# Performance work log

Hardware: AMD Instinct MI355X
Metric: run time of the kernel (lower is better)

Reference implementation:

```python
import jax, jax.numpy as jnp
import numpy as np

N_HEADS = 12
HEAD_DIM = 32
H_OUT = 28
W_OUT = 28
EPS_LN = 1e-6
EPS_TS = 1e-6


def _layer_norm(x, g, eps=EPS_LN):
    mu = jnp.mean(x, axis=-1, keepdims=True)
    xc = x - mu
    var = jnp.mean(xc * xc, axis=-1, keepdims=True)
    return xc * jax.lax.rsqrt(var + eps) * g


def setup_inputs() -> dict:
    key = jax.random.key(0)
    ks = jax.random.split(key, 6)
    b, hh, ww, d = 4, 56, 56, 384
    nc = 2 * H_OUT * W_OUT  # 1568
    s = 0.02
    return {
        "x": jax.random.normal(ks[0], (b, hh, ww, d), jnp.float32),
        "clusters": jax.random.normal(ks[1], (b, nc, d), jnp.float32),
        "g1": jnp.ones((d,), jnp.float32),
        "Wq": jax.random.normal(ks[2], (d, d), jnp.float32) * s,
        "Wkv": jax.random.normal(ks[3], (d, 2 * d), jnp.float32) * s,
        "Wo": jax.random.normal(ks[4], (d, d), jnp.float32) * s,
        "res_scale": jnp.ones((d,), jnp.float32),
        "g2": jnp.ones((2 * d,), jnp.float32),
        "Wproj": jax.random.normal(ks[5], (2 * d, 768), jnp.float32) * s,
    }


def reference(x, clusters, g1, Wq, Wkv, Wo, res_scale, g2, Wproj):
    b, hh, ww, d = x.shape
    n = hh * ww
    nc = clusters.shape[1]
    dh = HEAD_DIM
    scale = dh ** -0.5

    xf = x.reshape(b, n, d)
    xn = _layer_norm(xf, g1)
    cn = _layer_norm(clusters, g1)

    # projections; rearrange 'b n (h d) -> b h n d' and 'b n (k h d) -> k b h n d'
    q = (cn @ Wq).reshape(b, nc, N_HEADS, dh).transpose(0, 2, 1, 3)
    kv = (xn @ Wkv).reshape(b, n, 2, N_HEADS, dh)
    k = kv[:, :, 0].transpose(0, 2, 1, 3)  # [b h n dh]
    v = kv[:, :, 1].transpose(0, 2, 1, 3)

    attn = jnp.einsum('bhqd,bhkd->bhqk', q, k) * scale  # [b h nc n]
    # soft assignment: softmax over the query (cluster) axis
    attn = jax.nn.softmax(attn, axis=-2)
    token_sizes = attn.sum(-1)  # [b h nc]
    attn = attn / (token_sizes[..., None] + EPS_TS)
    token_sizes = token_sizes.mean(1)  # [b nc]

    c2 = jnp.einsum('bhqk,bhkd->bhqd', attn, v)
    c2 = c2.transpose(0, 2, 1, 3).reshape(b, nc, d) @ Wo

    token_sizes = token_sizes.reshape(b, nc // 2, 2).sum(-1)  # [b n']

    y = clusters * res_scale + c2
    y = y.reshape(b, nc // 2, 2 * d)  # 'b (n two) d -> b n (two d)'
    y = _layer_norm(y, g2) @ Wproj
    y = y.reshape(b, H_OUT, W_OUT, -1)
    token_sizes = token_sizes.reshape(b, H_OUT, W_OUT)
    return y, token_sizes
```

## Files before the change

### kernel.cpp

```cpp
#include <hip/hip_runtime.h>
#include <hip/hip_bf16.h>

typedef __hip_bfloat16 bf16;
typedef __attribute__((ext_vector_type(8))) short short8;
typedef __attribute__((ext_vector_type(4))) short short4v;
typedef __attribute__((ext_vector_type(4))) float f32x4;

#define B 4
#define NT 3136
#define NC 1568
#define NP 784
#define DMODEL 384
#define D2 768
#define NH 12
#define DH 32
#define SCALE 0.17677669529663687f
#define EPS_LN 1e-6f
#define EPS_TS 1e-6f

__device__ __forceinline__ unsigned short f2bf(float f) {
  return (unsigned short)(__bfloat16_as_ushort(__float2bfloat16(f)));
}
__device__ __forceinline__ float b2f(unsigned short u) {
  return __uint_as_float(((unsigned int)u) << 16);
}

__device__ __forceinline__ float lda(const void* __restrict__ p, size_t i,
                                     int mode, bool inf32) {
  bool f32 = (mode == 2) || (mode == 1 && inf32);
  return f32 ? ((const float*)p)[i]
             : __bfloat162float(((const bf16*)p)[i]);
}
__device__ __forceinline__ float4 lda4(const void* __restrict__ p, size_t i,
                                       int mode, bool inf32) {
  bool f32 = (mode == 2) || (mode == 1 && inf32);
  if (f32) return *(const float4*)((const float*)p + i);
  ushort4 u = *(const ushort4*)((const bf16*)p + i);
  return make_float4(b2f(u.x), b2f(u.y), b2f(u.z), b2f(u.w));
}

__global__ void sniff_kernel(const unsigned short* __restrict__ g1,
                             int* __restrict__ flag) {
  if (threadIdx.x == 0 && blockIdx.x == 0)
    *flag = (g1[0] == 0x3F80) ? 0 : 1;
}

__global__ void transpose_kernel(const void* __restrict__ in,
                                 const int* __restrict__ dtf,
                                 bf16* __restrict__ out, int K, int N) {
  bool inf32 = (*dtf != 0);
  __shared__ float t[32][33];
  int n0 = blockIdx.x * 32, k0 = blockIdx.y * 32;
  int tx = threadIdx.x & 31, ty = threadIdx.x >> 5;
#pragma unroll
  for (int s = 0; s < 32; s += 8)
    t[ty + s][tx] = lda(in, (size_t)(k0 + ty + s) * N + n0 + tx, 1, inf32);
  __syncthreads();
#pragma unroll
  for (int s = 0; s < 32; s += 8)
    out[(size_t)(n0 + ty + s) * K + k0 + tx] = __float2bfloat16(t[tx][ty + s]);
}

__global__ void stats_kernel(const void* __restrict__ in, int mode,
                             const int* __restrict__ dtf,
                             float* __restrict__ stats, int D) {
  bool inf32 = (*dtf != 0);
  int row = blockIdx.x;
  int tid = threadIdx.x;
  size_t base = (size_t)row * D;
  int nper = D >> 7;
  float s = 0.f, s2 = 0.f;
  for (int i = 0; i < nper; i++) {
    float xv = lda(in, base + tid + (i << 7), mode, inf32);
    s += xv; s2 += xv * xv;
  }
  __shared__ float red[128], red2[128];
  red[tid] = s; red2[tid] = s2;
  __syncthreads();
  for (int off = 64; off > 0; off >>= 1) {
    if (tid < off) { red[tid] += red[tid + off]; red2[tid] += red2[tid + off]; }
    __syncthreads();
  }
  if (tid == 0) {
    float mean = red[0] / (float)D;
    float var  = red2[0] / (float)D - mean * mean;
    stats[row * 2]     = mean;
    stats[row * 2 + 1] = rsqrtf(var + EPS_LN);
  }
}

__global__ void __launch_bounds__(256, 3)
mgemm_kernel(const void* __restrict__ A, int a_mode, size_t a_bstr,
             const float* __restrict__ Astats, size_t s_bstr,
             const void* __restrict__ gammaA,
             const bf16* __restrict__ BT,
             const int* __restrict__ dtf,
             void* __restrict__ C, int c_f32, size_t c_bstr,
             bf16* __restrict__ Cv,
             int M, int N, int K,
             int epi,
             const void* __restrict__ resid, size_t r_bstr,
             const void* __restrict__ rscale) {
  bool inf32 = (*dtf != 0);
  int z = blockIdx.z;
  size_t a_off = (size_t)z * a_bstr;
  size_t r_off = (size_t)z * r_bstr;
  const float* st = Astats ? Astats + (size_t)z * s_bstr : nullptr;
  __shared__ __align__(16) unsigned short Asl[128][40];
  __shared__ __align__(16) unsigned short Bsl[128][40];
  int tid = threadIdx.x;
  int wave = tid >> 6, lane = tid & 63, l16 = lane & 15, quad = lane >> 4;
  int brow = blockIdx.y * 128, bcol = blockIdx.x * 128;
  int wm = (wave >> 1) * 64, wn = (wave & 1) * 64;
  f32x4 acc[4][4];
#pragma unroll
  for (int i = 0; i < 4; i++)
#pragma unroll
    for (int j = 0; j < 4; j++) acc[i][j] = (f32x4){0.f, 0.f, 0.f, 0.f};

  for (int k0 = 0; k0 < K; k0 += 32) {
#pragma unroll
    for (int it = 0; it < 4; it++) {
      int i = it * 256 + tid;
      int r = i >> 3, c4 = (i & 7) * 4;
      int grow = brow + r;
      if (grow >= M) grow = M - 1;
      float4 v = lda4(A, a_off + (size_t)grow * K + k0 + c4, a_mode, inf32);
      if (st) {
        float mu = st[grow * 2], rstd = st[grow * 2 + 1];
        float4 g = lda4(gammaA, k0 + c4, 1, inf32);
        v.x = (v.x - mu) * rstd * g.x; v.y = (v.y - mu) * rstd * g.y;
        v.z = (v.z - mu) * rstd * g.z; v.w = (v.w - mu) * rstd * g.w;
      }
      ushort4 u = {f2bf(v.x), f2bf(v.y), f2bf(v.z), f2bf(v.w)};
      *(ushort4*)&Asl[r][c4] = u;
    }
#pragma unroll
    for (int it = 0; it < 4; it++) {
      int i = it * 256 + tid;
      int r = i >> 3, c4 = (i & 7) * 4;
      *(ushort4*)&Bsl[r][c4] =
          *(const ushort4*)(BT + (size_t)(bcol + r) * K + k0 + c4);
    }
    __syncthreads();
    short8 af[4], bfr[4];
#pragma unroll
    for (int i = 0; i < 4; i++)
      af[i] = *(const short8*)&Asl[wm + 16 * i + l16][quad * 8];
#pragma unroll
    for (int j = 0; j < 4; j++)
      bfr[j] = *(const short8*)&Bsl[wn + 16 * j + l16][quad * 8];
#pragma unroll
    for (int i = 0; i < 4; i++)
#pragma unroll
      for (int j = 0; j < 4; j++)
        acc[i][j] = __builtin_amdgcn_mfma_f32_16x16x32_bf16(
            af[i], bfr[j], acc[i][j], 0, 0, 0);
    __syncthreads();
  }
#pragma unroll
  for (int i = 0; i < 4; i++) {
#pragma unroll
    for (int r = 0; r < 4; r++) {
      int m = brow + wm + 16 * i + quad * 4 + r;
      if (m < M) {
#pragma unroll
        for (int j = 0; j < 4; j++) {
          int n = bcol + wn + 16 * j + l16;
          float v = acc[i][j][r];
          if (epi == 1)
            v += lda(resid, r_off + (size_t)m * N + n, 1, inf32) *
                 lda(rscale, n, 1, inf32);
          if (epi == 2) {
            if (n < DMODEL) {
              ((bf16*)C)[(size_t)z * c_bstr + (size_t)m * DMODEL + n] =
                  __float2bfloat16(v);
            } else {
              int cc = n - DMODEL, hh = cc >> 5, dd = cc & 31;
              Cv[(((size_t)z * NH + hh) * DH + dd) * NT + m] =
                  __float2bfloat16(v);
            }
          } else {
            size_t idx = (size_t)z * c_bstr + (size_t)m * N + n;
            if (c_f32) ((float*)C)[idx] = v;
            else       ((bf16*)C)[idx]  = __float2bfloat16(v);
          }
        }
      }
    }
  }
}

__global__ void __launch_bounds__(256, 4)
colsum_mfma(const bf16* __restrict__ qm, const bf16* __restrict__ km,
            float* __restrict__ csinv) {
  int b = blockIdx.z, h = blockIdx.y;
  int tid = threadIdx.x;
  int wave = tid >> 6, lane = tid & 63, l16 = lane & 15, quad = lane >> 4;
  int key = blockIdx.x * 64 + wave * 16 + l16;
  short8 kfrag = *(const short8*)(km +
      ((size_t)(b * NT + key) * DMODEL + h * DH + quad * 8));
  __shared__ __align__(16) unsigned short Qlds[32][40];
  const bf16* qb = qm + (size_t)b * NC * DMODEL + h * DH;
  int srow = tid >> 3, sc4 = (tid & 7) * 4;
  float csum = 0.f;
  for (int q0 = 0; q0 < NC; q0 += 32) {
    ushort4 qu = *(const ushort4*)(qb + (size_t)(q0 + srow) * DMODEL + sc4);
    __syncthreads();
    *(ushort4*)&Qlds[srow][sc4] = qu;
    __syncthreads();
    short8 a1 = *(const short8*)&Qlds[l16][quad * 8];
    short8 a2 = *(const short8*)&Qlds[16 + l16][quad * 8];
    f32x4 z = {0.f, 0.f, 0.f, 0.f};
    f32x4 s1 = __builtin_amdgcn_mfma_f32_16x16x32_bf16(a1, kfrag, z, 0, 0, 0);
    f32x4 s2 = __builtin_amdgcn_mfma_f32_16x16x32_bf16(a2, kfrag, z, 0, 0, 0);
#pragma unroll
    for (int r = 0; r < 4; r++)
      csum += __expf(s1[r] * SCALE) + __expf(s2[r] * SCALE);
  }
  csum += __shfl_xor(csum, 16, 64);
  csum += __shfl_xor(csum, 32, 64);
  if (quad == 0)
    csinv[((size_t)b * NH + h) * NT + key] = 1.0f / csum;
}

__global__ void __launch_bounds__(256, 4)
pv_mfma(const bf16* __restrict__ qm, const bf16* __restrict__ km,
        const bf16* __restrict__ vt, const float* __restrict__ csinv,
        bf16* __restrict__ c2, float* __restrict__ rowsum) {
  int b = blockIdx.z, h = blockIdx.y;
  int tid = threadIdx.x;
  int wave = tid >> 6, lane = tid & 63, l16 = lane & 15, quad = lane >> 4;
  int q0w = blockIdx.x * 128 + wave * 32;
  short8 qfrag[2];
#pragma unroll
  for (int t = 0; t < 2; t++) {
    int qr = q0w + t * 16 + l16; if (qr >= NC) qr = NC - 1;
    qfrag[t] = *(const short8*)(qm +
        ((size_t)(b * NC + qr) * DMODEL + h * DH + quad * 8));
  }
  __shared__ __align__(16) unsigned short Klds[64][40];
  __shared__ __align__(16) unsigned short Vlds[32][72];
  __shared__ __align__(16) float csl[64];
  f32x4 olo[2], ohi[2];
#pragma unroll
  for (int t = 0; t < 2; t++) {
    olo[t] = (f32x4){0.f, 0.f, 0.f, 0.f};
    ohi[t] = (f32x4){0.f, 0.f, 0.f, 0.f};
  }
  float rs[2] = {0.f, 0.f};
  const float* csb = csinv + ((size_t)b * NH + h) * NT;
  const bf16* kb = km + (size_t)b * NT * DMODEL + h * DH;
  const bf16* vtb = vt + ((size_t)b * NH + h) * DH * NT;
  int krow = tid >> 2, kc8 = (tid & 3) * 8;
  int vrow = tid >> 3, vc8 = (tid & 7) * 8;
  for (int k0 = 0; k0 < NT; k0 += 64) {
    ushort4 ku0 = *(const ushort4*)(kb + (size_t)(k0 + krow) * DMODEL + kc8);
    ushort4 ku1 = *(const ushort4*)(kb + (size_t)(k0 + krow) * DMODEL + kc8 + 4);
    ushort4 vu0 = *(const ushort4*)(vtb + (size_t)vrow * NT + k0 + vc8);
    ushort4 vu1 = *(const ushort4*)(vtb + (size_t)vrow * NT + k0 + vc8 + 4);
    float4 cf;
    if (tid < 16) cf = *(const float4*)(csb + k0 + tid * 4);
    __syncthreads();
    *(ushort4*)&Klds[krow][kc8] = ku0;
    *(ushort4*)&Klds[krow][kc8 + 4] = ku1;
    *(ushort4*)&Vlds[vrow][vc8] = vu0;
    *(ushort4*)&Vlds[vrow][vc8 + 4] = vu1;
    if (tid < 16) *(float4*)&csl[tid * 4] = cf;
    __syncthreads();
#pragma unroll
    for (int ks = 0; ks < 64; ks += 32) {
      short8 kf1 = *(const short8*)&Klds[ks + l16][quad * 8];
      short8 kf2 = *(const short8*)&Klds[ks + 16 + l16][quad * 8];
      float4 ci1 = *(const float4*)&csl[ks + quad * 4];
      float4 ci2 = *(const float4*)&csl[ks + 16 + quad * 4];
      short4v va = *(const short4v*)&Vlds[l16][ks + quad * 4];
      short4v vb = *(const short4v*)&Vlds[l16][ks + 16 + quad * 4];
      short4v vc = *(const short4v*)&Vlds[16 + l16][ks + quad * 4];
      short4v vd = *(const short4v*)&Vlds[16 + l16][ks + 16 + quad * 4];
      short8 vlo, vhi;
#pragma unroll
      for (int j = 0; j < 4; j++) {
        vlo[j] = va[j]; vlo[4 + j] = vb[j];
        vhi[j] = vc[j]; vhi[4 + j] = vd[j];
      }
#pragma unroll
      for (int t = 0; t < 2; t++) {
        f32x4 z = {0.f, 0.f, 0.f, 0.f};
        f32x4 s1 = __builtin_amdgcn_mfma_f32_16x16x32_bf16(kf1, qfrag[t], z, 0, 0, 0);
        f32x4 s2 = __builtin_amdgcn_mfma_f32_16x16x32_bf16(kf2, qfrag[t], z, 0, 0, 0);
        float p0 = __expf(s1[0] * SCALE) * ci1.x;
        float p1 = __expf(s1[1] * SCALE) * ci1.y;
        float p2 = __expf(s1[2] * SCALE) * ci1.z;
        float p3 = __expf(s1[3] * SCALE) * ci1.w;
        float p4 = __expf(s2[0] * SCALE) * ci2.x;
        float p5 = __expf(s2[1] * SCALE) * ci2.y;
        float p6 = __expf(s2[2] * SCALE) * ci2.z;
        float p7 = __expf(s2[3] * SCALE) * ci2.w;
        rs[t] += ((p0 + p1) + (p2 + p3)) + ((p4 + p5) + (p6 + p7));
        short8 pf;
        pf[0] = (short)f2bf(p0); pf[1] = (short)f2bf(p1);
        pf[2] = (short)f2bf(p2); pf[3] = (short)f2bf(p3);
        pf[4] = (short)f2bf(p4); pf[5] = (short)f2bf(p5);
        pf[6] = (short)f2bf(p6); pf[7] = (short)f2bf(p7);
        olo[t] = __builtin_amdgcn_mfma_f32_16x16x32_bf16(pf, vlo, olo[t], 0, 0, 0);
        ohi[t] = __builtin_amdgcn_mfma_f32_16x16x32_bf16(pf, vhi, ohi[t], 0, 0, 0);
      }
    }
  }
  bf16* c2b = c2 + (size_t)b * NC * DMODEL + h * DH;
#pragma unroll
  for (int t = 0; t < 2; t++) {
    float v = rs[t];
    v += __shfl_xor(v, 16, 64);
    v += __shfl_xor(v, 32, 64);
    rs[t] = v;
#pragma unroll
    for (int r = 0; r < 4; r++) {
      int qloc = quad * 4 + r;
      float rsq = __shfl(rs[t], qloc, 64);
      int q = q0w + t * 16 + qloc;
      if (q < NC) {
        float inv = 1.0f / (rsq + EPS_TS);
        c2b[(size_t)q * DMODEL + l16]      = __float2bfloat16(olo[t][r] * inv);
        c2b[(size_t)q * DMODEL + 16 + l16] = __float2bfloat16(ohi[t][r] * inv);
      }
    }
    int qr = q0w + t * 16 + l16;
    if (quad == 0 && qr < NC)
      rowsum[((size_t)b * NH + h) * NC + qr] = rs[t];
  }
}

__global__ void tok_kernel(const float* __restrict__ rowsum,
                           float* __restrict__ out_ts) {
  int idx = blockIdx.x * 256 + threadIdx.x;
  if (idx >= B * NP) return;
  int b = idx / NP, p = idx % NP;
  float s = 0.f;
  for (int h = 0; h < NH; h++) {
    const float* r = rowsum + ((size_t)b * NH + h) * NC;
    s += r[2 * p] + r[2 * p + 1];
  }
  out_ts[idx] = s / (float)NH;
}

extern "C" void kernel_launch(void* const* d_in, const int* in_sizes, int n_in,
                              void* d_out, int out_size, void* d_ws, size_t ws_size,
                              hipStream_t stream) {
  const void* x         = d_in[0];
  const void* clusters  = d_in[1];
  const void* g1        = d_in[2];
  const void* Wq        = d_in[3];
  const void* Wkv       = d_in[4];
  const void* Wo        = d_in[5];
  const void* res_scale = d_in[6];
  const void* g2        = d_in[7];
  const void* Wproj     = d_in[8];
  float* out = (float*)d_out;

  float* fws = (float*)d_ws;
  size_t fo = 0;
  int*   dtf     = (int*)(fws + fo); fo += 4;
  float* stats_x = fws + fo; fo += (size_t)B * NT * 2;
  float* stats_c = fws + fo; fo += (size_t)B * NC * 2;
  float* stats_y = fws + fo; fo += (size_t)B * NP * 2;
  float* colsum  = fws + fo; fo += (size_t)B * NH * NT;
  float* rowsum  = fws + fo; fo += (size_t)B * NH * NC;
  float* y1f     = fws + fo; fo += (size_t)B * NC * DMODEL;
  fo = (fo + 3) & ~(size_t)3;
  bf16* bws = (bf16*)(fws + fo);
  size_t o = 0;
  bf16* qm     = bws + o; o += (size_t)B * NC * DMODEL;
  bf16* km     = bws + o; o += (size_t)B * NT * DMODEL;
  bf16* vt     = bws + o; o += (size_t)B * NH * DH * NT;
  bf16* c2     = bws + o; o += (size_t)B * NC * DMODEL;
  bf16* wqT    = bws + o; o += (size_t)DMODEL * DMODEL;
  bf16* wkvT   = bws + o; o += (size_t)DMODEL * D2;
  bf16* woT    = bws + o; o += (size_t)DMODEL * DMODEL;
  bf16* wprojT = bws + o; o += (size_t)D2 * D2;

  const size_t xstr = (size_t)NT * DMODEL, cstr = (size_t)NC * DMODEL;
  const size_t ystr = (size_t)NP * D2;

  sniff_kernel<<<1, 1, 0, stream>>>((const unsigned short*)g1, dtf);
  transpose_kernel<<<dim3(DMODEL / 32, DMODEL / 32), 256, 0, stream>>>(
      Wq, dtf, wqT, DMODEL, DMODEL);
  transpose_kernel<<<dim3(D2 / 32, DMODEL / 32), 256, 0, stream>>>(
      Wkv, dtf, wkvT, DMODEL, D2);
  transpose_kernel<<<dim3(DMODEL / 32, DMODEL / 32), 256, 0, stream>>>(
      Wo, dtf, woT, DMODEL, DMODEL);
  transpose_kernel<<<dim3(D2 / 32, D2 / 32), 256, 0, stream>>>(
      Wproj, dtf, wprojT, D2, D2);
  stats_kernel<<<B * NT, 128, 0, stream>>>(x, 1, dtf, stats_x, DMODEL);
  stats_kernel<<<B * NC, 128, 0, stream>>>(clusters, 1, dtf, stats_c, DMODEL);

  mgemm_kernel<<<dim3(DMODEL / 128, (NC + 127) / 128, B), 256, 0, stream>>>(
      clusters, 1, cstr, stats_c, (size_t)NC * 2, g1, wqT, dtf,
      qm, 0, cstr, nullptr, NC, DMODEL, DMODEL, 0, nullptr, 0, nullptr);
  mgemm_kernel<<<dim3(D2 / 128, (NT + 127) / 128, B), 256, 0, stream>>>(
      x, 1, xstr, stats_x, (size_t)NT * 2, g1, wkvT, dtf,
      km, 0, xstr, vt, NT, D2, DMODEL, 2, nullptr, 0, nullptr);
  colsum_mfma<<<dim3(NT / 64, NH, B), 256, 0, stream>>>(qm, km, colsum);
  pv_mfma<<<dim3((NC + 127) / 128, NH, B), 256, 0, stream>>>(
      qm, km, vt, colsum, c2, rowsum);
  mgemm_kernel<<<dim3(DMODEL / 128, (NC + 127) / 128, B), 256, 0, stream>>>(
      c2, 0, cstr, nullptr, 0, nullptr, woT, dtf,
      y1f, 1, cstr, nullptr, NC, DMODEL, DMODEL, 1, clusters, cstr, res_scale);
  stats_kernel<<<B * NP, 128, 0, stream>>>(y1f, 2, dtf, stats_y, D2);
  mgemm_kernel<<<dim3(D2 / 128, (NP + 127) / 128, B), 256, 0, stream>>>(
      y1f, 2, cstr, stats_y, (size_t)NP * 2, g2, wprojT, dtf,
      out, 1, ystr, nullptr, NP, D2, D2, 0, nullptr, 0, nullptr);
  tok_kernel<<<(B * NP + 255) / 256, 256, 0, stream>>>(
      rowsum, out + (size_t)B * NP * D2);
}
```

Before: 443.4 us.

## Fold softmax scale into Wq, use exp2 with log-domain inverse, permute V layout

```diff
diff --git a/kernel.cpp b/kernel.cpp
--- a/kernel.cpp
+++ b/kernel.cpp
@@ -3,7 +3,6 @@
 
 typedef __hip_bfloat16 bf16;
 typedef __attribute__((ext_vector_type(8))) short short8;
-typedef __attribute__((ext_vector_type(4))) short short4v;
 typedef __attribute__((ext_vector_type(4))) float f32x4;
 
 #define B 4
@@ -15,6 +14,7 @@
 #define NH 12
 #define DH 32
 #define SCALE 0.17677669529663687f
+#define LOG2E 1.4426950408889634f
 #define EPS_LN 1e-6f
 #define EPS_TS 1e-6f
 
@@ -47,7 +47,8 @@
 
 __global__ void transpose_kernel(const void* __restrict__ in,
                                  const int* __restrict__ dtf,
-                                 bf16* __restrict__ out, int K, int N) {
+                                 bf16* __restrict__ out, int K, int N,
+                                 float scale) {
   bool inf32 = (*dtf != 0);
   __shared__ float t[32][33];
   int n0 = blockIdx.x * 32, k0 = blockIdx.y * 32;
@@ -58,7 +59,8 @@
   __syncthreads();
 #pragma unroll
   for (int s = 0; s < 32; s += 8)
-    out[(size_t)(n0 + ty + s) * K + k0 + tx] = __float2bfloat16(t[tx][ty + s]);
+    out[(size_t)(n0 + ty + s) * K + k0 + tx] =
+        __float2bfloat16(t[tx][ty + s] * scale);
 }
 
 __global__ void stats_kernel(const void* __restrict__ in, int mode,
@@ -177,7 +179,9 @@
                   __float2bfloat16(v);
             } else {
               int cc = n - DMODEL, hh = cc >> 5, dd = cc & 31;
-              Cv[(((size_t)z * NH + hh) * DH + dd) * NT + m] =
+              int w = m & 31;
+              int pos = ((w >> 2) & 3) * 8 + (w >> 4) * 4 + (w & 3);
+              Cv[(((size_t)z * NH + hh) * DH + dd) * NT + (m & ~31) + pos] =
                   __float2bfloat16(v);
             }
           } else {
@@ -193,17 +197,22 @@
 
 __global__ void __launch_bounds__(256, 4)
 colsum_mfma(const bf16* __restrict__ qm, const bf16* __restrict__ km,
-            float* __restrict__ csinv) {
+            float* __restrict__ l2ci) {
   int b = blockIdx.z, h = blockIdx.y;
   int tid = threadIdx.x;
   int wave = tid >> 6, lane = tid & 63, l16 = lane & 15, quad = lane >> 4;
-  int key = blockIdx.x * 64 + wave * 16 + l16;
-  short8 kfrag = *(const short8*)(km +
-      ((size_t)(b * NT + key) * DMODEL + h * DH + quad * 8));
+  int key0 = blockIdx.x * 128 + wave * 32 + l16;
+  int key1 = key0 + 16;
+  int kc0 = (key0 < NT) ? key0 : NT - 1;
+  int kc1 = (key1 < NT) ? key1 : NT - 1;
+  short8 kf0 = *(const short8*)(km +
+      ((size_t)(b * NT + kc0) * DMODEL + h * DH + quad * 8));
+  short8 kf1 = *(const short8*)(km +
+      ((size_t)(b * NT + kc1) * DMODEL + h * DH + quad * 8));
   __shared__ __align__(16) unsigned short Qlds[32][40];
   const bf16* qb = qm + (size_t)b * NC * DMODEL + h * DH;
   int srow = tid >> 3, sc4 = (tid & 7) * 4;
-  float csum = 0.f;
+  float cs0 = 0.f, cs1 = 0.f;
   for (int q0 = 0; q0 < NC; q0 += 32) {
     ushort4 qu = *(const ushort4*)(qb + (size_t)(q0 + srow) * DMODEL + sc4);
     __syncthreads();
@@ -212,21 +221,29 @@
     short8 a1 = *(const short8*)&Qlds[l16][quad * 8];
     short8 a2 = *(const short8*)&Qlds[16 + l16][quad * 8];
     f32x4 z = {0.f, 0.f, 0.f, 0.f};
-    f32x4 s1 = __builtin_amdgcn_mfma_f32_16x16x32_bf16(a1, kfrag, z, 0, 0, 0);
-    f32x4 s2 = __builtin_amdgcn_mfma_f32_16x16x32_bf16(a2, kfrag, z, 0, 0, 0);
-#pragma unroll
-    for (int r = 0; r < 4; r++)
-      csum += __expf(s1[r] * SCALE) + __expf(s2[r] * SCALE);
-  }
-  csum += __shfl_xor(csum, 16, 64);
-  csum += __shfl_xor(csum, 32, 64);
-  if (quad == 0)
-    csinv[((size_t)b * NH + h) * NT + key] = 1.0f / csum;
+    f32x4 s10 = __builtin_amdgcn_mfma_f32_16x16x32_bf16(a1, kf0, z, 0, 0, 0);
+    f32x4 s20 = __builtin_amdgcn_mfma_f32_16x16x32_bf16(a2, kf0, z, 0, 0, 0);
+    f32x4 s11 = __builtin_amdgcn_mfma_f32_16x16x32_bf16(a1, kf1, z, 0, 0, 0);
+    f32x4 s21 = __builtin_amdgcn_mfma_f32_16x16x32_bf16(a2, kf1, z, 0, 0, 0);
+#pragma unroll
+    for (int r = 0; r < 4; r++) {
+      cs0 += exp2f(s10[r]) + exp2f(s20[r]);
+      cs1 += exp2f(s11[r]) + exp2f(s21[r]);
+    }
+  }
+  cs0 += __shfl_xor(cs0, 16, 64);
+  cs0 += __shfl_xor(cs0, 32, 64);
+  cs1 += __shfl_xor(cs1, 16, 64);
+  cs1 += __shfl_xor(cs1, 32, 64);
+  if (quad == 0) {
+    if (key0 < NT) l2ci[((size_t)b * NH + h) * NT + key0] = -__log2f(cs0);
+    if (key1 < NT) l2ci[((size_t)b * NH + h) * NT + key1] = -__log2f(cs1);
+  }
 }
 
 __global__ void __launch_bounds__(256, 4)
 pv_mfma(const bf16* __restrict__ qm, const bf16* __restrict__ km,
-        const bf16* __restrict__ vt, const float* __restrict__ csinv,
+        const bf16* __restrict__ vt, const float* __restrict__ l2ci,
         bf16* __restrict__ c2, float* __restrict__ rowsum) {
   int b = blockIdx.z, h = blockIdx.y;
   int tid = threadIdx.x;
@@ -249,23 +266,19 @@
     ohi[t] = (f32x4){0.f, 0.f, 0.f, 0.f};
   }
   float rs[2] = {0.f, 0.f};
-  const float* csb = csinv + ((size_t)b * NH + h) * NT;
+  const float* csb = l2ci + ((size_t)b * NH + h) * NT;
   const bf16* kb = km + (size_t)b * NT * DMODEL + h * DH;
   const bf16* vtb = vt + ((size_t)b * NH + h) * DH * NT;
   int krow = tid >> 2, kc8 = (tid & 3) * 8;
   int vrow = tid >> 3, vc8 = (tid & 7) * 8;
   for (int k0 = 0; k0 < NT; k0 += 64) {
-    ushort4 ku0 = *(const ushort4*)(kb + (size_t)(k0 + krow) * DMODEL + kc8);
-    ushort4 ku1 = *(const ushort4*)(kb + (size_t)(k0 + krow) * DMODEL + kc8 + 4);
-    ushort4 vu0 = *(const ushort4*)(vtb + (size_t)vrow * NT + k0 + vc8);
-    ushort4 vu1 = *(const ushort4*)(vtb + (size_t)vrow * NT + k0 + vc8 + 4);
+    short8 ku = *(const short8*)(kb + (size_t)(k0 + krow) * DMODEL + kc8);
+    short8 vu = *(const short8*)(vtb + (size_t)vrow * NT + k0 + vc8);
     float4 cf;
     if (tid < 16) cf = *(const float4*)(csb + k0 + tid * 4);
     __syncthreads();
-    *(ushort4*)&Klds[krow][kc8] = ku0;
-    *(ushort4*)&Klds[krow][kc8 + 4] = ku1;
-    *(ushort4*)&Vlds[vrow][vc8] = vu0;
-    *(ushort4*)&Vlds[vrow][vc8 + 4] = vu1;
+    *(short8*)&Klds[krow][kc8] = ku;
+    *(short8*)&Vlds[vrow][vc8] = vu;
     if (tid < 16) *(float4*)&csl[tid * 4] = cf;
     __syncthreads();
 #pragma unroll
@@ -274,29 +287,21 @@
       short8 kf2 = *(const short8*)&Klds[ks + 16 + l16][quad * 8];
       float4 ci1 = *(const float4*)&csl[ks + quad * 4];
       float4 ci2 = *(const float4*)&csl[ks + 16 + quad * 4];
-      short4v va = *(const short4v*)&Vlds[l16][ks + quad * 4];
-      short4v vb = *(const short4v*)&Vlds[l16][ks + 16 + quad * 4];
-      short4v vc = *(const short4v*)&Vlds[16 + l16][ks + quad * 4];
-      short4v vd = *(const short4v*)&Vlds[16 + l16][ks + 16 + quad * 4];
-      short8 vlo, vhi;
-#pragma unroll
-      for (int j = 0; j < 4; j++) {
-        vlo[j] = va[j]; vlo[4 + j] = vb[j];
-        vhi[j] = vc[j]; vhi[4 + j] = vd[j];
-      }
+      short8 vlo = *(const short8*)&Vlds[l16][ks + quad * 8];
+      short8 vhi = *(const short8*)&Vlds[16 + l16][ks + quad * 8];
 #pragma unroll
       for (int t = 0; t < 2; t++) {
         f32x4 z = {0.f, 0.f, 0.f, 0.f};
         f32x4 s1 = __builtin_amdgcn_mfma_f32_16x16x32_bf16(kf1, qfrag[t], z, 0, 0, 0);
         f32x4 s2 = __builtin_amdgcn_mfma_f32_16x16x32_bf16(kf2, qfrag[t], z, 0, 0, 0);
-        float p0 = __expf(s1[0] * SCALE) * ci1.x;
-        float p1 = __expf(s1[1] * SCALE) * ci1.y;
-        float p2 = __expf(s1[2] * SCALE) * ci1.z;
-        float p3 = __expf(s1[3] * SCALE) * ci1.w;
-        float p4 = __expf(s2[0] * SCALE) * ci2.x;
-        float p5 = __expf(s2[1] * SCALE) * ci2.y;
-        float p6 = __expf(s2[2] * SCALE) * ci2.z;
-        float p7 = __expf(s2[3] * SCALE) * ci2.w;
+        float p0 = exp2f(s1[0] + ci1.x);
+        float p1 = exp2f(s1[1] + ci1.y);
+        float p2 = exp2f(s1[2] + ci1.z);
+        float p3 = exp2f(s1[3] + ci1.w);
+        float p4 = exp2f(s2[0] + ci2.x);
+        float p5 = exp2f(s2[1] + ci2.y);
+        float p6 = exp2f(s2[2] + ci2.z);
+        float p7 = exp2f(s2[3] + ci2.w);
         rs[t] += ((p0 + p1) + (p2 + p3)) + ((p4 + p5) + (p6 + p7));
         short8 pf;
         pf[0] = (short)f2bf(p0); pf[1] = (short)f2bf(p1);
@@ -385,13 +390,13 @@
 
   sniff_kernel<<<1, 1, 0, stream>>>((const unsigned short*)g1, dtf);
   transpose_kernel<<<dim3(DMODEL / 32, DMODEL / 32), 256, 0, stream>>>(
-      Wq, dtf, wqT, DMODEL, DMODEL);
+      Wq, dtf, wqT, DMODEL, DMODEL, SCALE * LOG2E);
   transpose_kernel<<<dim3(D2 / 32, DMODEL / 32), 256, 0, stream>>>(
-      Wkv, dtf, wkvT, DMODEL, D2);
+      Wkv, dtf, wkvT, DMODEL, D2, 1.0f);
   transpose_kernel<<<dim3(DMODEL / 32, DMODEL / 32), 256, 0, stream>>>(
-      Wo, dtf, woT, DMODEL, DMODEL);
+      Wo, dtf, woT, DMODEL, DMODEL, 1.0f);
   transpose_kernel<<<dim3(D2 / 32, D2 / 32), 256, 0, stream>>>(
-      Wproj, dtf, wprojT, D2, D2);
+      Wproj, dtf, wprojT, D2, D2, 1.0f);
   stats_kernel<<<B * NT, 128, 0, stream>>>(x, 1, dtf, stats_x, DMODEL);
   stats_kernel<<<B * NC, 128, 0, stream>>>(clusters, 1, dtf, stats_c, DMODEL);
 
@@ -401,7 +406,7 @@
   mgemm_kernel<<<dim3(D2 / 128, (NT + 127) / 128, B), 256, 0, stream>>>(
       x, 1, xstr, stats_x, (size_t)NT * 2, g1, wkvT, dtf,
       km, 0, xstr, vt, NT, D2, DMODEL, 2, nullptr, 0, nullptr);
-  colsum_mfma<<<dim3(NT / 64, NH, B), 256, 0, stream>>>(qm, km, colsum);
+  colsum_mfma<<<dim3((NT + 127) / 128, NH, B), 256, 0, stream>>>(qm, km, colsum);
   pv_mfma<<<dim3((NC + 127) / 128, NH, B), 256, 0, stream>>>(
       qm, km, vt, colsum, c2, rowsum);
   mgemm_kernel<<<dim3(DMODEL / 128, (NC + 127) / 128, B), 256, 0, stream>>>(
```

New measurement: 480.8 us. 1.08x slower.
